# Optimization experiments

Hardware: AMD Instinct MI355X
Metric: run time of the kernel (lower is better)

Reference implementation:

```python
import jax, jax.numpy as jnp
import numpy as np

K_SIZE = 3
STRIDE = 1
PAD = 1


def _extract_patches(X, k, stride, pad):
    """X: [N,H,W,C] -> patches [N,Ho,Wo,k*k*C], ordered (dh, dw, c) to match
    filters.reshape(c_out, k*k*C)."""
    Xp = jnp.pad(X, ((0, 0), (pad, pad), (pad, pad), (0, 0)))
    N, Hp, Wp, C = Xp.shape
    Ho = (Hp - k) // stride + 1
    Wo = (Wp - k) // stride + 1
    slabs = [Xp[:, dh:dh + stride * Ho:stride, dw:dw + stride * Wo:stride, :]
             for dh in range(k) for dw in range(k)]  # fixed small k*k loop
    P = jnp.stack(slabs, axis=3)  # [N,Ho,Wo,k*k,C]
    return P.reshape(N, Ho, Wo, k * k * C)


def setup_inputs() -> dict:
    key = jax.random.key(0)
    k1, k2 = jax.random.split(key)
    X = jax.random.normal(k1, (8, 32, 32, 32), dtype=jnp.float32)
    filters = jax.random.normal(k2, (64, 3, 3, 32), dtype=jnp.float32)
    return {"X": X, "filters": filters}


def reference(X, filters):
    # AdderNet forward: Z[n,h,w,f] = sum_{dh,dw,c} |window(n,h,w) - filters[f]|
    c_out = filters.shape[0]
    P = _extract_patches(X, K_SIZE, STRIDE, PAD)  # [N,Ho,Wo,K]
    N, Ho, Wo, K = P.shape
    F = filters.reshape(c_out, K)
    # L1 distance between every patch and every filter: [M, c_out]
    D = jnp.abs(P.reshape(-1, 1, K) - F[None, :, :]).sum(axis=-1)
    return D.reshape(N, Ho, Wo, c_out)
```

## Files before the change

### kernel.cpp

```cpp
#include <hip/hip_runtime.h>


#define BLOCK 256

__global__ __launch_bounds__(256, 4) void adder_fwd(const float* __restrict__ X,
                                                    const float* __restrict__ Fg,
                                                    float* __restrict__ out) {
    __shared__ float Xs[3 * 18 * 32];

    const int b  = blockIdx.x;
    const int fh = b & 1;
    const int wh = (b >> 1) & 1;
    const int h  = (b >> 2) & 31;
    const int n  = b >> 7;
    const int w0 = wh * 16;
    const int tid = threadIdx.x;

    const int lane = tid & 63;
    const int c8   = lane & 7;
    const int f    = lane >> 3;
    const int wave = __builtin_amdgcn_readfirstlane(tid >> 6);
    const int f0   = fh * 32 + wave * 8;
    const int fid  = f0 + f;

    float4 fr[9];
    {
        const float* fp = Fg + (size_t)fid * 288 + c8 * 4;
        #pragma unroll
        for (int t = 0; t < 9; ++t)
            fr[t] = *(const float4*)(fp + t * 32);
    }

    #pragma unroll
    for (int it = 0; it < 2; ++it) {
        int idx = tid + BLOCK * it;
        if (idx < 432) {
            int c4  = idx & 7;
            int t   = idx >> 3;
            int col = t % 18;
            int row = t / 18;
            int hr  = h + row - 1;
            int gw  = w0 + col - 1;
            float4 v = make_float4(0.f, 0.f, 0.f, 0.f);
            if ((unsigned)hr < 32u && (unsigned)gw < 32u)
                v = ((const float4*)(X + (((size_t)n * 32 + hr) * 32 + gw) * 32))[c4];
            ((float4*)(Xs + (row * 18 + col) * 32))[c4] = v;
        }
    }
    __syncthreads();

    const float* xb = Xs + c8 * 4;
    const size_t obase = (((size_t)n * 32 + h) * 32 + w0) * 64 + fid;

    #pragma unroll 1
    for (int pg = 0; pg < 4; ++pg) {
        float4 acc[4];
        #pragma unroll
        for (int pp = 0; pp < 4; ++pp)
            acc[pp] = make_float4(0.f, 0.f, 0.f, 0.f);

        #pragma unroll
        for (int dh = 0; dh < 3; ++dh) {
            float4 x[6];
            #pragma unroll
            for (int j = 0; j < 6; ++j)
                x[j] = *(const float4*)(xb + (dh * 18 + pg * 4 + j) * 32);

            #pragma unroll
            for (int dw = 0; dw < 3; ++dw) {
                const float4 fv = fr[dh * 3 + dw];
                #pragma unroll
                for (int pp = 0; pp < 4; ++pp) {
                    const float4 xv = x[pp + dw];
                    acc[pp].x += fabsf(xv.x - fv.x);
                    acc[pp].y += fabsf(xv.y - fv.y);
                    acc[pp].z += fabsf(xv.z - fv.z);
                    acc[pp].w += fabsf(xv.w - fv.w);
                }
            }
        }

        float s0 = (acc[0].x + acc[0].y) + (acc[0].z + acc[0].w);
        float s1 = (acc[1].x + acc[1].y) + (acc[1].z + acc[1].w);
        float s2 = (acc[2].x + acc[2].y) + (acc[2].z + acc[2].w);
        float s3 = (acc[3].x + acc[3].y) + (acc[3].z + acc[3].w);

        s0 += __shfl_xor(s0, 1, 64);  s1 += __shfl_xor(s1, 1, 64);
        s2 += __shfl_xor(s2, 1, 64);  s3 += __shfl_xor(s3, 1, 64);
        s0 += __shfl_xor(s0, 2, 64);  s1 += __shfl_xor(s1, 2, 64);
        s2 += __shfl_xor(s2, 2, 64);  s3 += __shfl_xor(s3, 2, 64);
        s0 += __shfl_xor(s0, 4, 64);  s1 += __shfl_xor(s1, 4, 64);
        s2 += __shfl_xor(s2, 4, 64);  s3 += __shfl_xor(s3, 4, 64);

        if (c8 < 4) {
            float v = s0;
            if (c8 == 1) v = s1;
            else if (c8 == 2) v = s2;
            else if (c8 == 3) v = s3;
            out[obase + (size_t)(pg * 4 + c8) * 64] = v;
        }
    }
}

extern "C" void kernel_launch(void* const* d_in, const int* in_sizes, int n_in,
                              void* d_out, int out_size, void* d_ws, size_t ws_size,
                              hipStream_t stream) {
    const float* X = (const float*)d_in[0];
    const float* F = (const float*)d_in[1];
    float* out = (float*)d_out;
    adder_fwd<<<dim3(1024), dim3(256), 0, stream>>>(X, F, out);
}
```

Measured before the change: 63.73 us.

## Use 512-thread blocks covering all filters, double-buffer LDS loads, DPP reductions

```diff
diff --git a/kernel.cpp b/kernel.cpp
--- a/kernel.cpp
+++ b/kernel.cpp
@@ -1,18 +1,23 @@
 #include <hip/hip_runtime.h>
 
 
-#define BLOCK 256
+#define BLOCK 512
 
-__global__ __launch_bounds__(256, 4) void adder_fwd(const float* __restrict__ X,
+template <int CTRL>
+__device__ __forceinline__ float dpp_add(float s) {
+    int t = __builtin_amdgcn_update_dpp(0, __float_as_int(s), CTRL, 0xf, 0xf, true);
+    return s + __int_as_float(t);
+}
+
+__global__ __launch_bounds__(512, 4) void adder_fwd(const float* __restrict__ X,
                                                     const float* __restrict__ Fg,
                                                     float* __restrict__ out) {
     __shared__ float Xs[3 * 18 * 32];
 
     const int b  = blockIdx.x;
-    const int fh = b & 1;
-    const int wh = (b >> 1) & 1;
-    const int h  = (b >> 2) & 31;
-    const int n  = b >> 7;
+    const int wh = b & 1;
+    const int h  = (b >> 1) & 31;
+    const int n  = b >> 6;
     const int w0 = wh * 16;
     const int tid = threadIdx.x;
 
@@ -20,8 +25,7 @@
     const int c8   = lane & 7;
     const int f    = lane >> 3;
     const int wave = __builtin_amdgcn_readfirstlane(tid >> 6);
-    const int f0   = fh * 32 + wave * 8;
-    const int fid  = f0 + f;
+    const int fid  = wave * 8 + f;
 
     float4 fr[9];
     {
@@ -31,75 +35,87 @@
             fr[t] = *(const float4*)(fp + t * 32);
     }
 
-    #pragma unroll
-    for (int it = 0; it < 2; ++it) {
-        int idx = tid + BLOCK * it;
-        if (idx < 432) {
-            int c4  = idx & 7;
-            int t   = idx >> 3;
-            int col = t % 18;
-            int row = t / 18;
-            int hr  = h + row - 1;
-            int gw  = w0 + col - 1;
-            float4 v = make_float4(0.f, 0.f, 0.f, 0.f);
-            if ((unsigned)hr < 32u && (unsigned)gw < 32u)
-                v = ((const float4*)(X + (((size_t)n * 32 + hr) * 32 + gw) * 32))[c4];
-            ((float4*)(Xs + (row * 18 + col) * 32))[c4] = v;
-        }
+    if (tid < 432) {
+        int c4  = tid & 7;
+        int t   = tid >> 3;
+        int col = t % 18;
+        int row = t / 18;
+        int hr  = h + row - 1;
+        int gw  = w0 + col - 1;
+        float4 v = make_float4(0.f, 0.f, 0.f, 0.f);
+        if ((unsigned)hr < 32u && (unsigned)gw < 32u)
+            v = ((const float4*)(X + (((size_t)n * 32 + hr) * 32 + gw) * 32))[c4];
+        ((float4*)(Xs + (row * 18 + col) * 32))[c4] = v;
     }
     __syncthreads();
 
     const float* xb = Xs + c8 * 4;
     const size_t obase = (((size_t)n * 32 + h) * 32 + w0) * 64 + fid;
 
-    #pragma unroll 1
-    for (int pg = 0; pg < 4; ++pg) {
-        float4 acc[4];
-        #pragma unroll
-        for (int pp = 0; pp < 4; ++pp)
-            acc[pp] = make_float4(0.f, 0.f, 0.f, 0.f);
+    float4 xA[6], xB[6], acc[4];
 
-        #pragma unroll
-        for (int dh = 0; dh < 3; ++dh) {
-            float4 x[6];
-            #pragma unroll
-            for (int j = 0; j < 6; ++j)
-                x[j] = *(const float4*)(xb + (dh * 18 + pg * 4 + j) * 32);
+#define LD(dst, dh, col0)                                                   \
+    {                                                                       \
+        _Pragma("unroll")                                                   \
+        for (int j = 0; j < 6; ++j)                                         \
+            dst[j] = *(const float4*)(xb + ((dh) * 18 + (col0) + j) * 32);  \
+    }
 
-            #pragma unroll
-            for (int dw = 0; dw < 3; ++dw) {
-                const float4 fv = fr[dh * 3 + dw];
-                #pragma unroll
-                for (int pp = 0; pp < 4; ++pp) {
-                    const float4 xv = x[pp + dw];
-                    acc[pp].x += fabsf(xv.x - fv.x);
-                    acc[pp].y += fabsf(xv.y - fv.y);
-                    acc[pp].z += fabsf(xv.z - fv.z);
-                    acc[pp].w += fabsf(xv.w - fv.w);
-                }
-            }
-        }
+#define COMP(xx, t0)                                                        \
+    {                                                                       \
+        _Pragma("unroll")                                                   \
+        for (int dw = 0; dw < 3; ++dw) {                                    \
+            const float4 fv = fr[(t0) + dw];                                \
+            _Pragma("unroll")                                               \
+            for (int pp = 0; pp < 4; ++pp) {                                \
+                const float4 xv = xx[pp + dw];                              \
+                acc[pp].x += fabsf(xv.x - fv.x);                            \
+                acc[pp].y += fabsf(xv.y - fv.y);                            \
+                acc[pp].z += fabsf(xv.z - fv.z);                            \
+                acc[pp].w += fabsf(xv.w - fv.w);                            \
+            }                                                               \
+        }                                                                   \
+    }
 
-        float s0 = (acc[0].x + acc[0].y) + (acc[0].z + acc[0].w);
-        float s1 = (acc[1].x + acc[1].y) + (acc[1].z + acc[1].w);
-        float s2 = (acc[2].x + acc[2].y) + (acc[2].z + acc[2].w);
-        float s3 = (acc[3].x + acc[3].y) + (acc[3].z + acc[3].w);
+#define PG(pg, B0, B1, LAST)                                                \
+    {                                                                       \
+        _Pragma("unroll")                                                   \
+        for (int pp = 0; pp < 4; ++pp)                                      \
+            acc[pp] = make_float4(0.f, 0.f, 0.f, 0.f);                      \
+        LD(B1, 1, (pg) * 4);                                \
+        COMP(B0, 0);                                      \
+        LD(B0, 2, (pg) * 4);                                \
+        COMP(B1, 3);                                      \
+        if (!(LAST)) LD(B1, 0, ((pg) + 1) * 4);         \
+        COMP(B0, 6);                                      \
+        float s0 = (acc[0].x + acc[0].y) + (acc[0].z + acc[0].w);           \
+        float s1 = (acc[1].x + acc[1].y) + (acc[1].z + acc[1].w);           \
+        float s2 = (acc[2].x + acc[2].y) + (acc[2].z + acc[2].w);           \
+        float s3 = (acc[3].x + acc[3].y) + (acc[3].z + acc[3].w);           \
+        s0 = dpp_add<0xB1>(s0);  s1 = dpp_add<0xB1>(s1);                    \
+        s2 = dpp_add<0xB1>(s2);  s3 = dpp_add<0xB1>(s3);                    \
+        s0 = dpp_add<0x4E>(s0);  s1 = dpp_add<0x4E>(s1);                    \
+        s2 = dpp_add<0x4E>(s2);  s3 = dpp_add<0x4E>(s3);                    \
+        s0 = dpp_add<0x141>(s0); s1 = dpp_add<0x141>(s1);                   \
+        s2 = dpp_add<0x141>(s2); s3 = dpp_add<0x141>(s3);                   \
+        if (c8 < 4) {                                                       \
+            float v = s0;                                                   \
+            if (c8 == 1) v = s1;                                            \
+            else if (c8 == 2) v = s2;                                       \
+            else if (c8 == 3) v = s3;                                       \
+            out[obase + (size_t)((pg) * 4 + c8) * 64] = v;                  \
+        }                                                                   \
+    }
 
-        s0 += __shfl_xor(s0, 1, 64);  s1 += __shfl_xor(s1, 1, 64);
-        s2 += __shfl_xor(s2, 1, 64);  s3 += __shfl_xor(s3, 1, 64);
-        s0 += __shfl_xor(s0, 2, 64);  s1 += __shfl_xor(s1, 2, 64);
-        s2 += __shfl_xor(s2, 2, 64);  s3 += __shfl_xor(s3, 2, 64);
-        s0 += __shfl_xor(s0, 4, 64);  s1 += __shfl_xor(s1, 4, 64);
-        s2 += __shfl_xor(s2, 4, 64);  s3 += __shfl_xor(s3, 4, 64);
+    LD(xA, 0, 0);
+    PG(0, xA, xB, 0)
+    PG(1, xB, xA, 0)
+    PG(2, xA, xB, 0)
+    PG(3, xB, xA, 1)
 
-        if (c8 < 4) {
-            float v = s0;
-            if (c8 == 1) v = s1;
-            else if (c8 == 2) v = s2;
-            else if (c8 == 3) v = s3;
-            out[obase + (size_t)(pg * 4 + c8) * 64] = v;
-        }
-    }
+#undef PG
+#undef COMP
+#undef LD
 }
 
 extern "C" void kernel_launch(void* const* d_in, const int* in_sizes, int n_in,
@@ -108,5 +124,5 @@
     const float* X = (const float*)d_in[0];
     const float* F = (const float*)d_in[1];
     float* out = (float*)d_out;
-    adder_fwd<<<dim3(1024), dim3(256), 0, stream>>>(X, F, out);
+    adder_fwd<<<dim3(512), dim3(512), 0, stream>>>(X, F, out);
 }
```

Measured after the change: 62.40 us, median of 2. -2.1%, faster.
